# Kernel optimization log

Hardware: AMD Instinct MI355X
Metric: run time of the kernel (lower is better)

## Reference

```python
import jax, jax.numpy as jnp
import numpy as np
import math

K = 8          # wavelet order (k)
C = 64         # channels (c)
ICH = 512      # ich = c*k
ALPHA = 16     # fourier modes
BATCH, SEQ, NH, NE = 4, 3072, 8, 64   # x: [B, L, H, E], H*E == ICH


def _legendre_filters(k):
    # numpy port of FiSSM/FEDformer get_filter(base='legendre', k): PHI0=PHI1=I
    from numpy.polynomial import legendre as npl, polynomial as npp
    phi_c = np.zeros((k, k)); phi2_c = np.zeros((k, k))
    for ki in range(k):
        e = np.zeros(ki + 1); e[ki] = 1.0
        pc = npl.leg2poly(e)                                  # P_ki power coeffs
        p = npp.Polynomial(pc)(npp.Polynomial([-1.0, 2.0]))
        phi_c[ki, :len(p.coef)] = np.sqrt(2 * ki + 1) * p.coef
        p2 = npp.Polynomial(pc)(npp.Polynomial([-1.0, 4.0]))
        phi2_c[ki, :len(p2.coef)] = np.sqrt(2.0) * np.sqrt(2 * ki + 1) * p2.coef

    def _int_half(prod, upper_half):
        prod = prod.copy(); prod[np.abs(prod) < 1e-8] = 0
        n = np.arange(len(prod))
        w = (1 - np.power(0.5, 1 + n)) if upper_half else np.power(0.5, 1 + n)
        return (prod / (n + 1) * w).sum()

    psi1_c = np.zeros((k, k)); psi2_c = np.zeros((k, k))
    for ki in range(k):
        psi1_c[ki] = phi2_c[ki]
        for i in range(k):
            proj = _int_half(np.convolve(phi2_c[ki, :ki + 1], phi_c[i, :i + 1]), False)
            psi1_c[ki] -= proj * phi_c[i]
            psi2_c[ki] -= proj * phi_c[i]
        for j in range(ki):
            proj = _int_half(np.convolve(phi2_c[ki, :ki + 1], psi1_c[j]), False)
            psi1_c[ki] -= proj * psi1_c[j]
            psi2_c[ki] -= proj * psi2_c[j]
        norm1 = _int_half(np.convolve(psi1_c[ki], psi1_c[ki]), False)
        norm2 = _int_half(np.convolve(psi2_c[ki], psi2_c[ki]), True)
        nrm = np.sqrt(norm1 + norm2)
        psi1_c[ki] /= nrm; psi2_c[ki] /= nrm
        psi1_c[np.abs(psi1_c) < 1e-8] = 0; psi2_c[np.abs(psi2_c) < 1e-8] = 0

    nodes, weights = np.polynomial.legendre.leggauss(k)
    xm = (nodes + 1) / 2; wm = weights / 2     # Gauss-Legendre on [0,1]
    pv = np.polynomial.polynomial.polyval
    phi = lambda i, t: pv(t, phi_c[i])
    psi = lambda i, t: np.where(t <= 0.5, pv(t, psi1_c[i]), pv(t, psi2_c[i]))
    H0 = np.zeros((k, k)); H1 = np.zeros((k, k)); G0 = np.zeros((k, k)); G1 = np.zeros((k, k))
    r2 = 1 / np.sqrt(2)
    for ki in range(k):
        for kp in range(k):
            base = wm * phi(kp, xm)
            H0[ki, kp] = r2 * (base * phi(ki, xm / 2)).sum()
            G0[ki, kp] = r2 * (base * psi(ki, xm / 2)).sum()
            H1[ki, kp] = r2 * (base * phi(ki, (xm + 1) / 2)).sum()
            G1[ki, kp] = r2 * (base * psi(ki, (xm + 1) / 2)).sum()
    for M in (H0, H1, G0, G1):
        M[np.abs(M) < 1e-8] = 0
    ec_s = np.concatenate([H0.T, H1.T], 0).astype(np.float32)   # [2k, k]
    ec_d = np.concatenate([G0.T, G1.T], 0).astype(np.float32)
    rc_e = np.concatenate([H0, G0], 0).astype(np.float32)       # H0r=H0@I etc.
    rc_o = np.concatenate([H1, G1], 0).astype(np.float32)
    return ec_s, ec_d, rc_e, rc_o


def _skft(x, wr, wi):
    # sparseKernelFT2d: FFT-domain conv over the sequence axis, low `modes1` bins
    B, L, c, k = x.shape
    xv = x.reshape(B, L, c * k).transpose(0, 2, 1)     # [B, ck, L]
    xf = jnp.fft.rfft(xv)                              # [B, ck, L//2+1]
    nf = L // 2 + 1
    l = min(wr.shape[-1], nf)
    w = jax.lax.complex(wr[:, :, :l], wi[:, :, :l])
    out = jnp.einsum('bix,iox->box', xf[:, :, :l], w)
    out_ft = jnp.zeros((B, c * k, nf), dtype=out.dtype).at[:, :, :l].set(out)
    y = jnp.fft.irfft(out_ft, n=L)                     # torch default n == L (L even here)
    return y.transpose(0, 2, 1).reshape(B, L, c, k)


def _forward(x, Lk0_w, Lk0_b, Lk1_w, Lk1_b, T0_w, T0_b, Ar, Ai, Br, Bi, Cr, Ci, ec_s, ec_d, rc_e, rc_o):
    B, L, H, E = x.shape
    v = x.reshape(B, L, H * E) @ Lk0_w.T + Lk0_b       # Lk0: ich -> c*k
    v = v.reshape(B, L, C, K)
    # --- MWT_CZ2d (nCZ = 1, level offset self.L = 0) ---
    ns = int(math.floor(math.log2(L)))
    nl = 2 ** int(math.ceil(math.log2(L)))
    v = jnp.concatenate([v, v[:, :nl - L]], axis=1)    # circular-style pad to 2^ceil
    Ud, Us = [], []
    for _ in range(ns):                                # wavelet decompose
        xa = jnp.concatenate([v[:, ::2], v[:, 1::2]], axis=-1)   # [B, N/2, c, 2k]
        d = xa @ ec_d
        v = xa @ ec_s
        Ud.append(_skft(d, Ar, Ai) + _skft(v, Br, Bi))
        Us.append(_skft(d, Cr, Ci))
    v = v @ T0_w.T + T0_b                              # T0 on coarsest scale
    for i in range(ns - 1, -1, -1):                    # evenOdd reconstruct
        v = v + Us[i]
        ve = jnp.concatenate([v, Ud[i]], axis=-1)      # [B, N, c, 2k]
        xe = ve @ rc_e
        xo = ve @ rc_o
        v = jnp.stack([xe, xo], axis=2).reshape(xe.shape[0], 2 * xe.shape[1], C, K)
    v = v[:, :L]
    out = v.reshape(B, L, C * K) @ Lk1_w.T + Lk1_b     # Lk1: c*k -> ich
    return out.reshape(B, L, -1, E)


def setup_inputs():
    key = jax.random.key(0)
    ks = jax.random.split(key, 13)
    ck = C * K
    x = jax.random.normal(ks[0], (BATCH, SEQ, NH, NE), jnp.float32)
    l0 = 1.0 / math.sqrt(ICH)
    l1 = 1.0 / math.sqrt(ck)
    lt = 1.0 / math.sqrt(K)
    scale = 1.0 / (ck * ck)
    u = lambda k_, shp, lo, hi: jax.random.uniform(k_, shp, jnp.float32, lo, hi)
    inp = dict(
        x=x,
        Lk0_w=u(ks[1], (ck, ICH), -l0, l0), Lk0_b=u(ks[2], (ck,), -l0, l0),
        Lk1_w=u(ks[3], (ICH, ck), -l1, l1), Lk1_b=u(ks[4], (ICH,), -l1, l1),
        T0_w=u(ks[5], (K, K), -lt, lt), T0_b=u(ks[6], (K,), -lt, lt),
        Ar=scale * u(ks[7], (ck, ck, ALPHA), 0.0, 1.0), Ai=scale * u(ks[8], (ck, ck, ALPHA), 0.0, 1.0),
        Br=scale * u(ks[9], (ck, ck, ALPHA), 0.0, 1.0), Bi=scale * u(ks[10], (ck, ck, ALPHA), 0.0, 1.0),
        Cr=scale * u(ks[11], (ck, ck, ALPHA), 0.0, 1.0), Ci=scale * u(ks[12], (ck, ck, ALPHA), 0.0, 1.0),
    )
    ec_s, ec_d, rc_e, rc_o = _legendre_filters(K)
    inp.update(ec_s=jnp.asarray(ec_s), ec_d=jnp.asarray(ec_d),
               rc_e=jnp.asarray(rc_e), rc_o=jnp.asarray(rc_o))
    return inp


def reference(x, Lk0_w, Lk0_b, Lk1_w, Lk1_b, T0_w, T0_b, Ar, Ai, Br, Bi, Cr, Ci, ec_s, ec_d, rc_e, rc_o):
    return _forward(x, Lk0_w, Lk0_b, Lk1_w, Lk1_b, T0_w, T0_b,
                    Ar, Ai, Br, Bi, Cr, Ci, ec_s, ec_d, rc_e, rc_o)
```

## Files before the change

### kernel.cpp

```cpp
#include <hip/hip_runtime.h>

#define CKD 512
#define NROWS 44
#define XPLANE 360448

static __device__ __forceinline__ int imin(int a, int b) { return a < b ? a : b; }

typedef short bf16x8 __attribute__((ext_vector_type(8)));
typedef float f32x4 __attribute__((ext_vector_type(4)));
typedef unsigned int uint32;
typedef unsigned short ushort16;

static __device__ __forceinline__ unsigned int pk2(float a, float b) {
  unsigned int ua = __float_as_uint(a), ub = __float_as_uint(b);
  ua = (ua + 0x7fffu + ((ua >> 16) & 1u)) >> 16;
  ub = (ub + 0x7fffu + ((ub >> 16) & 1u)) >> 16;
  return ua | (ub << 16);
}

static __device__ __forceinline__ uint32 ror16(uint32 q) { return (q >> 16) | (q << 16); }

static __device__ __forceinline__ bf16x8 mk_neghi(uint32 q0, uint32 q1, uint32 q2, uint32 q3) {
  union { uint32 u[4]; bf16x8 h; } t;
  t.u[0] = q0 ^ 0x80000000u; t.u[1] = q1 ^ 0x80000000u;
  t.u[2] = q2 ^ 0x80000000u; t.u[3] = q3 ^ 0x80000000u;
  return t.h;
}
static __device__ __forceinline__ bf16x8 mk_swap(uint32 q0, uint32 q1, uint32 q2, uint32 q3) {
  union { uint32 u[4]; bf16x8 h; } t;
  t.u[0] = ror16(q0); t.u[1] = ror16(q1); t.u[2] = ror16(q2); t.u[3] = ror16(q3);
  return t.h;
}

__global__ __launch_bounds__(256) void k_cvt_x(
    const float* __restrict__ src, unsigned short* __restrict__ dst)
{
  int g = blockIdx.x * 256 + threadIdx.x;
  int row = g >> 6, c8 = (g & 63) << 3;
  int b = row >> 12, t = row & 4095;
  if (t >= 3072) t -= 3072;
  const float* s = src + ((size_t)(b * 3072 + t) << 9) + c8;
  float4 v0 = *(const float4*)s;
  float4 v1 = *(const float4*)(s + 4);
  uint4 o = make_uint4(pk2(v0.x, v0.y), pk2(v0.z, v0.w),
                       pk2(v1.x, v1.y), pk2(v1.z, v1.w));
  *(uint4*)(dst + ((size_t)row << 9) + c8) = o;
}

__global__ __launch_bounds__(256) void k_cvt_gen(
    const float* __restrict__ src, unsigned short* __restrict__ dst)
{
  int g = blockIdx.x * 256 + threadIdx.x;
  const float* s = src + ((size_t)g << 3);
  float4 v0 = *(const float4*)s;
  float4 v1 = *(const float4*)(s + 4);
  uint4 o = make_uint4(pk2(v0.x, v0.y), pk2(v0.z, v0.w),
                       pk2(v1.x, v1.y), pk2(v1.z, v1.w));
  *(uint4*)(dst + ((size_t)g << 3)) = o;
}

__global__ __launch_bounds__(256) void k_cvt_c(
    const float* __restrict__ src, unsigned short* __restrict__ dst)
{
  int g = blockIdx.x * 256 + threadIdx.x;
  int row = g >> 6, c8 = (g & 63) << 3;
  int b = row / 3072, t = row - b * 3072;
  const float* s = src + ((size_t)((b << 12) + t) << 9) + c8;
  float4 v0 = *(const float4*)s;
  float4 v1 = *(const float4*)(s + 4);
  uint4 o = make_uint4(pk2(v0.x, v0.y), pk2(v0.z, v0.w),
                       pk2(v1.x, v1.y), pk2(v1.z, v1.w));
  *(uint4*)(dst + ((size_t)row << 9) + c8) = o;
}

__global__ __launch_bounds__(256) void k_gemm_bf16(
    const unsigned short* __restrict__ A, const unsigned short* __restrict__ W,
    const float* __restrict__ bias, float* __restrict__ Out)
{
  __shared__ unsigned short As[128 * 40];
  __shared__ unsigned short Bs[128 * 40];
  const int tid = threadIdx.x;
  const int row = tid >> 1, half = tid & 1;
  const int bm0 = blockIdx.x << 7, bn0 = blockIdx.y << 7;
  const int wv = tid >> 6, l = tid & 63;
  const int wm0 = (wv & 1) << 6, wn0 = (wv >> 1) << 6;
  const int fr = l & 15, fq = l >> 4;

  const unsigned short* Ap = A + (size_t)(bm0 + row) * CKD + half * 16;
  const unsigned short* Wp = W + (size_t)(bn0 + row) * CKD + half * 16;

  f32x4 acc[4][4];
#pragma unroll
  for (int mt = 0; mt < 4; ++mt)
#pragma unroll
    for (int nt = 0; nt < 4; ++nt) {
      acc[mt][nt][0] = 0.f; acc[mt][nt][1] = 0.f;
      acc[mt][nt][2] = 0.f; acc[mt][nt][3] = 0.f;
    }

  for (int k0 = 0; k0 < CKD; k0 += 32) {
    uint4 av0 = *(const uint4*)(Ap + k0);
    uint4 av1 = *(const uint4*)(Ap + k0 + 8);
    uint4 bv0 = *(const uint4*)(Wp + k0);
    uint4 bv1 = *(const uint4*)(Wp + k0 + 8);
    __syncthreads();
    *(uint4*)&As[row * 40 + half * 16]     = av0;
    *(uint4*)&As[row * 40 + half * 16 + 8] = av1;
    *(uint4*)&Bs[row * 40 + half * 16]     = bv0;
    *(uint4*)&Bs[row * 40 + half * 16 + 8] = bv1;
    __syncthreads();
    bf16x8 af[4], bfr[4];
#pragma unroll
    for (int mt = 0; mt < 4; ++mt)
      af[mt] = *(const bf16x8*)&As[(wm0 + mt * 16 + fr) * 40 + fq * 8];
#pragma unroll
    for (int nt = 0; nt < 4; ++nt)
      bfr[nt] = *(const bf16x8*)&Bs[(wn0 + nt * 16 + fr) * 40 + fq * 8];
#pragma unroll
    for (int mt = 0; mt < 4; ++mt)
#pragma unroll
      for (int nt = 0; nt < 4; ++nt)
        acc[mt][nt] = __builtin_amdgcn_mfma_f32_16x16x32_bf16(
            af[mt], bfr[nt], acc[mt][nt], 0, 0, 0);
  }

#pragma unroll
  for (int nt = 0; nt < 4; ++nt) {
    int col = bn0 + wn0 + nt * 16 + fr;
    float bv = bias[col];
#pragma unroll
    for (int mt = 0; mt < 4; ++mt) {
      int r0 = bm0 + wm0 + mt * 16 + fq * 4;
#pragma unroll
      for (int rg = 0; rg < 4; ++rg)
        Out[(size_t)(r0 + rg) * CKD + col] = acc[mt][nt][rg] + bv;
    }
  }
}

__global__ __launch_bounds__(256) void k_decomp(
    const float* __restrict__ Vin, const float* __restrict__ ec_s,
    const float* __restrict__ ec_d, float* __restrict__ Dout,
    float* __restrict__ Vout, int Lout, int pin)
{
  __shared__ float Es[128], Ed[128];
  if (threadIdx.x < 128) Es[threadIdx.x] = ec_s[threadIdx.x];
  else Ed[threadIdx.x - 128] = ec_d[threadIdx.x - 128];
  __syncthreads();
  int g = blockIdx.x * 256 + threadIdx.x;
  if (g >= 4 * Lout * 64) return;
  int c = g & 63;
  int s = (g >> 6) % Lout;
  int b = g / (Lout << 6);
  const float* r0 = Vin + ((size_t)b * pin + 2 * s) * CKD + (c << 3);
  float a[16];
  float4 v0 = *(const float4*)r0;
  float4 v1 = *(const float4*)(r0 + 4);
  float4 v2 = *(const float4*)(r0 + CKD);
  float4 v3 = *(const float4*)(r0 + CKD + 4);
  a[0]=v0.x; a[1]=v0.y; a[2]=v0.z; a[3]=v0.w; a[4]=v1.x; a[5]=v1.y; a[6]=v1.z; a[7]=v1.w;
  a[8]=v2.x; a[9]=v2.y; a[10]=v2.z; a[11]=v2.w; a[12]=v3.x; a[13]=v3.y; a[14]=v3.z; a[15]=v3.w;
  float dv[8] = {}, vv[8] = {};
#pragma unroll
  for (int m = 0; m < 16; ++m)
#pragma unroll
    for (int k = 0; k < 8; ++k) {
      dv[k] += a[m] * Ed[m * 8 + k];
      vv[k] += a[m] * Es[m * 8 + k];
    }
  size_t orow = ((size_t)b * Lout + s) * CKD + (c << 3);
  *(float4*)(Dout + orow)     = make_float4(dv[0], dv[1], dv[2], dv[3]);
  *(float4*)(Dout + orow + 4) = make_float4(dv[4], dv[5], dv[6], dv[7]);
  *(float4*)(Vout + orow)     = make_float4(vv[0], vv[1], vv[2], vv[3]);
  *(float4*)(Vout + orow + 4) = make_float4(vv[4], vv[5], vv[6], vv[7]);
}

__global__ __launch_bounds__(256) void k_t0(
    const float* __restrict__ Vin, const float* __restrict__ T0w,
    const float* __restrict__ T0b, float* __restrict__ Out)
{
  int g = blockIdx.x * 256 + threadIdx.x;
  if (g >= 4 * 2 * 64) return;
  int c = g & 63;
  int t = (g >> 6) & 1;
  int b = g >> 7;
  const float* src = Vin + ((size_t)(b * 2 + t)) * CKD + (c << 3);
  float a[8];
  float4 v0 = *(const float4*)src;
  float4 v1 = *(const float4*)(src + 4);
  a[0]=v0.x; a[1]=v0.y; a[2]=v0.z; a[3]=v0.w; a[4]=v1.x; a[5]=v1.y; a[6]=v1.z; a[7]=v1.w;
  float o[8];
#pragma unroll
  for (int ko = 0; ko < 8; ++ko) {
    float sum = T0b[ko];
#pragma unroll
    for (int k = 0; k < 8; ++k) sum += a[k] * T0w[ko * 8 + k];
    o[ko] = sum;
  }
  float* dst = Out + ((size_t)(b * 2 + t)) * CKD + (c << 3);
  *(float4*)dst       = make_float4(o[0], o[1], o[2], o[3]);
  *(float4*)(dst + 4) = make_float4(o[4], o[5], o[6], o[7]);
}

__global__ __launch_bounds__(256) void k_fdft(
    const float* __restrict__ DD, const float* __restrict__ VD,
    float* __restrict__ XDre, float* __restrict__ XDim,
    float* __restrict__ XVre, float* __restrict__ XVim)
{
  __shared__ float2 tw[2048];
  int bx = blockIdx.x, j = 1;
  for (;;) {
    int c = (4096 >> j) >> 7; if (c < 1) c = 1;
    if (bx < c) break;
    bx -= c; ++j;
  }
  const int L = 4096 >> j;
  const int t0 = bx << 7;
  const int tcnt = imin(128, L - t0);
  const int b = blockIdx.y;
  const int z = blockIdx.z;
  const int r = (j - 1) * 4 + b;
  const float* src = (z ? VD : DD) +
      ((size_t)(4 * (4096 - (4096 >> (j - 1))) + b * L)) * CKD;
  float* dre = z ? XVre : XDre;
  float* dim_ = z ? XVim : XDim;

  for (int idx = threadIdx.x; idx < 2048; idx += 256) {
    int ff = idx >> 7, tl = idx & 127;
    int t = t0 + tl;
    int m = (2 * ff * t) & (2 * L - 1);
    float xang = (float)m / (float)L;
    tw[idx] = make_float2(cospif(xang), sinpif(xang));
  }
  __syncthreads();

  float ar[16][2] = {};
  float ai[16][2] = {};
  const float* sp = src + (size_t)t0 * CKD + (threadIdx.x << 1);
  for (int tl = 0; tl < tcnt; ++tl) {
    float2 xv = *(const float2*)sp;
    sp += CKD;
#pragma unroll
    for (int ff = 0; ff < 16; ++ff) {
      float2 cs = tw[(ff << 7) + tl];
      ar[ff][0] += xv.x * cs.x; ar[ff][1] += xv.y * cs.x;
      ai[ff][0] -= xv.x * cs.y; ai[ff][1] -= xv.y * cs.y;
    }
  }
  const int i0 = threadIdx.x << 1;
#pragma unroll
  for (int ff = 0; ff < 16; ++ff) {
    size_t bidx = ((size_t)ff * NROWS + r) * CKD + i0;
    atomicAdd(&dre[bidx], ar[ff][0]);
    atomicAdd(&dre[bidx + 1], ar[ff][1]);
    atomicAdd(&dim_[bidx], ai[ff][0]);
    atomicAdd(&dim_[bidx + 1], ai[ff][1]);
  }
}

__global__ __launch_bounds__(256) void k_transw6b(
    const float* __restrict__ sAr, const float* __restrict__ sAi,
    const float* __restrict__ sBr, const float* __restrict__ sBi,
    const float* __restrict__ sCr, const float* __restrict__ sCi,
    uint2* __restrict__ W4b, uint32* __restrict__ W2b)
{
  int g = blockIdx.x * 256 + threadIdx.x;
  float ar[16], ai[16], br[16], bi[16], cr[16], ci[16];
  const size_t sb = (size_t)g * 16;
#pragma unroll
  for (int q = 0; q < 4; ++q) {
    float4 t;
    t = *(const float4*)(sAr + sb + q * 4); ar[q*4]=t.x; ar[q*4+1]=t.y; ar[q*4+2]=t.z; ar[q*4+3]=t.w;
    t = *(const float4*)(sAi + sb + q * 4); ai[q*4]=t.x; ai[q*4+1]=t.y; ai[q*4+2]=t.z; ai[q*4+3]=t.w;
    t = *(const float4*)(sBr + sb + q * 4); br[q*4]=t.x; br[q*4+1]=t.y; br[q*4+2]=t.z; br[q*4+3]=t.w;
    t = *(const float4*)(sBi + sb + q * 4); bi[q*4]=t.x; bi[q*4+1]=t.y; bi[q*4+2]=t.z; bi[q*4+3]=t.w;
    t = *(const float4*)(sCr + sb + q * 4); cr[q*4]=t.x; cr[q*4+1]=t.y; cr[q*4+2]=t.z; cr[q*4+3]=t.w;
    t = *(const float4*)(sCi + sb + q * 4); ci[q*4]=t.x; ci[q*4+1]=t.y; ci[q*4+2]=t.z; ci[q*4+3]=t.w;
  }
#pragma unroll
  for (int f = 0; f < 16; ++f) {
    size_t e = ((size_t)f << 18) + g;
    W4b[e] = make_uint2(pk2(ar[f], ai[f]), pk2(br[f], bi[f]));
    W2b[e] = pk2(cr[f], ci[f]);
  }
}

__global__ __launch_bounds__(256) void k_packA(
    const float* __restrict__ XDre, const float* __restrict__ XDim,
    const float* __restrict__ XVre, const float* __restrict__ XVim,
    unsigned short* __restrict__ Aud, unsigned short* __restrict__ Aus)
{
  int g = blockIdx.x * 256 + threadIdx.x;
  int f = g / 6144;
  int rem = g - f * 6144;
  int r = rem >> 7, iq = rem & 127;
  uint4 w0 = make_uint4(0,0,0,0), w1 = w0, wu = w0;
  if (r < NROWS) {
    size_t base = ((size_t)f * NROWS + r) * CKD + (iq << 2);
    float4 dre = *(const float4*)(XDre + base);
    float4 dim_ = *(const float4*)(XDim + base);
    float4 vre = *(const float4*)(XVre + base);
    float4 vim = *(const float4*)(XVim + base);
    w0 = make_uint4(pk2(dre.x, dim_.x), pk2(vre.x, vim.x),
                    pk2(dre.y, dim_.y), pk2(vre.y, vim.y));
    w1 = make_uint4(pk2(dre.z, dim_.z), pk2(vre.z, vim.z),
                    pk2(dre.w, dim_.w), pk2(vre.w, vim.w));
    wu = make_uint4(pk2(dre.x, dim_.x), pk2(dre.y, dim_.y),
                    pk2(dre.z, dim_.z), pk2(dre.w, dim_.w));
  }
  size_t du = ((size_t)f * 48 + r) * 2048 + (iq << 4);
  *(uint4*)(Aud + du)     = w0;
  *(uint4*)(Aud + du + 8) = w1;
  *(uint4*)(Aus + ((size_t)f * 48 + r) * 1024 + (iq << 3)) = wu;
}

__global__ __launch_bounds__(256) void k_mixmm(
    const uint2* __restrict__ W4b, const uint32* __restrict__ W2b,
    const unsigned short* __restrict__ Aud, const unsigned short* __restrict__ Aus,
    float* __restrict__ Part)
{
  __shared__ __attribute__((aligned(16))) uint2 sBud[16 * 130];
  __shared__ __attribute__((aligned(16))) uint32 sBus[16 * 132];
  __shared__ __attribute__((aligned(16))) unsigned short sAud[48 * 72];
  __shared__ __attribute__((aligned(16))) unsigned short sAus[48 * 40];

  const int f = blockIdx.x;
  const int o0 = blockIdx.y << 7;
  const int is = blockIdx.z;
  const int i0 = is << 7;
  const int tid = threadIdx.x;
  const int w = tid >> 6, l = tid & 63;
  const int fr = l & 15, fq = l >> 4;
  const int ow0 = w << 5;

  const uint2* gW4 = W4b + ((size_t)f << 18);
  const uint32* gW2 = W2b + ((size_t)f << 18);
  const unsigned short* gAud = Aud + (size_t)f * 48 * 2048;
  const unsigned short* gAus = Aus + (size_t)f * 48 * 1024;

  f32x4 aUd[3][2][2], aUs[3][2][2];
#pragma unroll
  for (int m = 0; m < 3; ++m)
#pragma unroll
    for (int ot = 0; ot < 2; ++ot)
#pragma unroll
      for (int cp = 0; cp < 2; ++cp) {
        aUd[m][ot][cp][0]=0.f; aUd[m][ot][cp][1]=0.f; aUd[m][ot][cp][2]=0.f; aUd[m][ot][cp][3]=0.f;
        aUs[m][ot][cp][0]=0.f; aUs[m][ot][cp][1]=0.f; aUs[m][ot][cp][2]=0.f; aUs[m][ot][cp][3]=0.f;
      }

  for (int ic = 0; ic < 8; ++ic) {
    const int ig = i0 + (ic << 4);
    __syncthreads();
#pragma unroll
    for (int n = 0; n < 4; ++n) {
      int q = tid + (n << 8);
      int il = q >> 6, op = (q & 63) << 1;
      uint4 v = *(const uint4*)(gW4 + (size_t)(ig + il) * 512 + o0 + op);
      *(uint4*)&sBud[il * 130 + op] = v;
    }
#pragma unroll
    for (int n = 0; n < 2; ++n) {
      int q = tid + (n << 8);
      int il = q >> 5, oq = (q & 31) << 2;
      uint4 v = *(const uint4*)(gW2 + (size_t)(ig + il) * 512 + o0 + oq);
      *(uint4*)&sBus[il * 132 + oq] = v;
    }
    {
      int q = tid;
      int m = q >> 3, k8 = (q & 7) << 3;
      uint4 v = *(const uint4*)(gAud + (size_t)m * 2048 + (is << 9) + (ic << 6) + k8);
      *(uint4*)&sAud[m * 72 + k8] = v;
      q = tid + 256;
      if (q < 384) {
        m = q >> 3; k8 = (q & 7) << 3;
        uint4 v2 = *(const uint4*)(gAud + (size_t)m * 2048 + (is << 9) + (ic << 6) + k8);
        *(uint4*)&sAud[m * 72 + k8] = v2;
      }
    }
    if (tid < 192) {
      int m = tid >> 2, k8 = (tid & 3) << 3;
      uint4 v = *(const uint4*)(gAus + (size_t)m * 1024 + (is << 8) + (ic << 5) + k8);
      *(uint4*)&sAus[m * 40 + k8] = v;
    }
    __syncthreads();

#pragma unroll
    for (int ks = 0; ks < 2; ++ks) {
      bf16x8 af[3];
#pragma unroll
      for (int m = 0; m < 3; ++m)
        af[m] = *(const bf16x8*)&sAud[(m * 16 + fr) * 72 + (ks << 5) + (fq << 3)];
#pragma unroll
      for (int ot = 0; ot < 2; ++ot) {
        int ol = ow0 + (ot << 4) + fr;
        int il = (ks << 3) + (fq << 1);
        uint2 qa = sBud[il * 130 + ol];
        uint2 qb = sBud[(il + 1) * 130 + ol];
        bf16x8 b0 = mk_neghi(qa.x, qa.y, qb.x, qb.y);
        bf16x8 b1 = mk_swap(qa.x, qa.y, qb.x, qb.y);
#pragma unroll
        for (int m = 0; m < 3; ++m) {
          aUd[m][ot][0] = __builtin_amdgcn_mfma_f32_16x16x32_bf16(af[m], b0, aUd[m][ot][0], 0, 0, 0);
          aUd[m][ot][1] = __builtin_amdgcn_mfma_f32_16x16x32_bf16(af[m], b1, aUd[m][ot][1], 0, 0, 0);
        }
      }
    }
    {
      bf16x8 af[3];
#pragma unroll
      for (int m = 0; m < 3; ++m)
        af[m] = *(const bf16x8*)&sAus[(m * 16 + fr) * 40 + (fq << 3)];
#pragma unroll
      for (int ot = 0; ot < 2; ++ot) {
        int ol = ow0 + (ot << 4) + fr;
        int il = fq << 2;
        uint32 q0 = sBus[(il + 0) * 132 + ol];
        uint32 q1 = sBus[(il + 1) * 132 + ol];
        uint32 q2 = sBus[(il + 2) * 132 + ol];
        uint32 q3 = sBus[(il + 3) * 132 + ol];
        bf16x8 b0 = mk_neghi(q0, q1, q2, q3);
        bf16x8 b1 = mk_swap(q0, q1, q2, q3);
#pragma unroll
        for (int m = 0; m < 3; ++m) {
          aUs[m][ot][0] = __builtin_amdgcn_mfma_f32_16x16x32_bf16(af[m], b0, aUs[m][ot][0], 0, 0, 0);
          aUs[m][ot][1] = __builtin_amdgcn_mfma_f32_16x16x32_bf16(af[m], b1, aUs[m][ot][1], 0, 0, 0);
        }
      }
    }
  }

  float* P = Part + (size_t)is * 4 * XPLANE;
#pragma unroll
  for (int m = 0; m < 3; ++m) {
#pragma unroll
    for (int reg = 0; reg < 4; ++reg) {
      int r = m * 16 + (fq << 2) + reg;
      if (r < NROWS) {
        size_t rb = ((size_t)f * NROWS + r) * CKD;
#pragma unroll
        for (int ot = 0; ot < 2; ++ot) {
          int col = o0 + ow0 + (ot << 4) + fr;
          P[0 * XPLANE + rb + col] = aUd[m][ot][0][reg];
          P[1 * XPLANE + rb + col] = aUd[m][ot][1][reg];
          P[2 * XPLANE + rb + col] = aUs[m][ot][0][reg];
          P[3 * XPLANE + rb + col] = aUs[m][ot][1][reg];
        }
      }
    }
  }
}

__global__ __launch_bounds__(256) void k_reduce4(
    const float* __restrict__ Part,
    float* __restrict__ UdFre, float* __restrict__ UdFim,
    float* __restrict__ UsFre, float* __restrict__ UsFim)
{
  int idx = blockIdx.x * 256 + threadIdx.x;
  if (idx >= XPLANE) return;
  float s0 = 0.f, s1 = 0.f, s2 = 0.f, s3 = 0.f;
#pragma unroll
  for (int is = 0; is < 4; ++is) {
    const float* p = Part + (size_t)is * 4 * XPLANE;
    s0 += p[0 * XPLANE + idx];
    s1 += p[1 * XPLANE + idx];
    s2 += p[2 * XPLANE + idx];
    s3 += p[3 * XPLANE + idx];
  }
  UdFre[idx] = s0; UdFim[idx] = s1; UsFre[idx] = s2; UsFim[idx] = s3;
}

__global__ __launch_bounds__(512) void k_mix_fb(
    const float* __restrict__ XDre, const float* __restrict__ XDim,
    const float* __restrict__ XVre, const float* __restrict__ XVim,
    const float* __restrict__ war, const float* __restrict__ wai,
    const float* __restrict__ wbr, const float* __restrict__ wbi,
    const float* __restrict__ wcr, const float* __restrict__ wci,
    float* __restrict__ UdFre, float* __restrict__ UdFim,
    float* __restrict__ UsFre, float* __restrict__ UsFim)
{
  const int f = blockIdx.x;
  const int ot = blockIdx.y;
  const int lane = threadIdx.x & 63;
  const int rg = threadIdx.x >> 6;
  const int rbase = (rg < 4) ? rg * 6 : 24 + (rg - 4) * 5;
  const int rcnt = (rg < 4) ? 6 : 5;
  const int o0 = (ot << 7) + lane;
  __shared__ float4 sx[NROWS * 64];
  float udr[6][2] = {}, udi[6][2] = {}, usr[6][2] = {}, usi[6][2] = {};
  for (int i0 = 0; i0 < 512; i0 += 64) {
    __syncthreads();
    for (int idx = threadIdx.x; idx < NROWS * 64; idx += 512) {
      int r = idx >> 6, il = idx & 63;
      size_t xb = ((size_t)f * NROWS + r) * CKD + i0 + il;
      sx[idx] = make_float4(XDre[xb], XDim[xb], XVre[xb], XVim[xb]);
    }
    __syncthreads();
    for (int ii = 0; ii < 64; ++ii) {
      int i = i0 + ii;
      size_t wo = ((((size_t)i << 9) + o0) << 4) + f;
      float4 wa0 = make_float4(war[wo], wai[wo], wbr[wo], wbi[wo]);
      float2 wc0 = make_float2(wcr[wo], wci[wo]);
      size_t w1 = wo + (64u << 4);
      float4 wa1 = make_float4(war[w1], wai[w1], wbr[w1], wbi[w1]);
      float2 wc1 = make_float2(wcr[w1], wci[w1]);
#pragma unroll
      for (int rr = 0; rr < 6; ++rr) {
        if (rr < rcnt) {
          float4 xv = sx[((rbase + rr) << 6) + ii];
          udr[rr][0] += xv.x * wa0.x - xv.y * wa0.y + xv.z * wa0.z - xv.w * wa0.w;
          udi[rr][0] += xv.x * wa0.y + xv.y * wa0.x + xv.z * wa0.w + xv.w * wa0.z;
          usr[rr][0] += xv.x * wc0.x - xv.y * wc0.y;
          usi[rr][0] += xv.x * wc0.y + xv.y * wc0.x;
          udr[rr][1] += xv.x * wa1.x - xv.y * wa1.y + xv.z * wa1.z - xv.w * wa1.w;
          udi[rr][1] += xv.x * wa1.y + xv.y * wa1.x + xv.z * wa1.w + xv.w * wa1.z;
          usr[rr][1] += xv.x * wc1.x - xv.y * wc1.y;
          usi[rr][1] += xv.x * wc1.y + xv.y * wc1.x;
        }
      }
    }
  }
#pragma unroll
  for (int rr = 0; rr < 6; ++rr) {
    if (rr < rcnt) {
      size_t rb_ = ((size_t)f * NROWS + rbase + rr) * CKD;
      UdFre[rb_ + o0] = udr[rr][0];      UdFre[rb_ + o0 + 64] = udr[rr][1];
      UdFim[rb_ + o0] = udi[rr][0];      UdFim[rb_ + o0 + 64] = udi[rr][1];
      UsFre[rb_ + o0] = usr[rr][0];      UsFre[rb_ + o0 + 64] = usr[rr][1];
      UsFim[rb_ + o0] = usi[rr][0];      UsFim[rb_ + o0 + 64] = usi[rr][1];
    }
  }
}

__global__ __launch_bounds__(256) void k_idft(
    const float* __restrict__ UdFre, const float* __restrict__ UdFim,
    const float* __restrict__ UsFre, const float* __restrict__ UsFim,
    float* __restrict__ UdT, float* __restrict__ UsT)
{
  __shared__ float2 tw[128];
  int bx = blockIdx.x, j = 1;
  for (;;) {
    int c = (4096 >> j) >> 3; if (c < 1) c = 1;
    if (bx < c) break;
    bx -= c; ++j;
  }
  const int L = 4096 >> j;
  const int l = imin(16, (L >> 1) + 1);
  const int t0 = bx << 3;
  const int b = blockIdx.y;
  const int r = (j - 1) * 4 + b;
  if (threadIdx.x < 128) {
    int ff = threadIdx.x >> 3, tl = threadIdx.x & 7;
    int t = t0 + tl;
    int m = (2 * ff * t) & (2 * L - 1);
    float xang = (float)m / (float)L;
    float wgt = (ff == 0 || 2 * ff == L) ? 1.0f : 2.0f;
    float sc = wgt / (float)L;
    tw[threadIdx.x] = make_float2(cospif(xang) * sc, sinpif(xang) * sc);
  }
  __syncthreads();
  const int o = threadIdx.x << 1;
  float2 ud[8], us[8];
#pragma unroll
  for (int tl = 0; tl < 8; ++tl) { ud[tl] = make_float2(0.f, 0.f); us[tl] = make_float2(0.f, 0.f); }
  for (int ff = 0; ff < l; ++ff) {
    size_t bidx = ((size_t)ff * NROWS + r) * CKD + o;
    float2 er = *(const float2*)(UdFre + bidx);
    float2 ei = *(const float2*)(UdFim + bidx);
    float2 sr = *(const float2*)(UsFre + bidx);
    float2 si = *(const float2*)(UsFim + bidx);
#pragma unroll
    for (int tl = 0; tl < 8; ++tl) {
      float2 cs = tw[(ff << 3) + tl];
      ud[tl].x += er.x * cs.x - ei.x * cs.y;
      ud[tl].y += er.y * cs.x - ei.y * cs.y;
      us[tl].x += sr.x * cs.x - si.x * cs.y;
      us[tl].y += sr.y * cs.x - si.y * cs.y;
    }
  }
  int tmax = imin(8, L - t0);
  size_t obase = ((size_t)(4 * (4096 - (4096 >> (j - 1))) + b * L + t0)) * CKD + o;
  for (int tl = 0; tl < tmax; ++tl) {
    *(float2*)(UdT + obase + (size_t)tl * CKD) = ud[tl];
    *(float2*)(UsT + obase + (size_t)tl * CKD) = us[tl];
  }
}

__global__ __launch_bounds__(256) void k_recon(
    const float* __restrict__ Vcur, const float* __restrict__ UdT,
    const float* __restrict__ UsT, const float* __restrict__ rc_e,
    const float* __restrict__ rc_o, float* __restrict__ Vnext,
    int Lc, int abase)
{
  __shared__ float Re[128], Ro[128];
  if (threadIdx.x < 128) Re[threadIdx.x] = rc_e[threadIdx.x];
  else Ro[threadIdx.x - 128] = rc_o[threadIdx.x - 128];
  __syncthreads();
  int g = blockIdx.x * 256 + threadIdx.x;
  if (g >= 4 * Lc * 64) return;
  int c = g & 63;
  int s = (g >> 6) % Lc;
  int b = g / (Lc << 6);
  size_t vrow = ((size_t)b * Lc + s) * CKD + (c << 3);
  size_t arow = ((size_t)abase + (size_t)b * Lc + s) * CKD + (c << 3);
  float a[16];
  {
    float4 t0_ = *(const float4*)(Vcur + vrow);
    float4 t1_ = *(const float4*)(Vcur + vrow + 4);
    float4 u0 = *(const float4*)(UsT + arow);
    float4 u1 = *(const float4*)(UsT + arow + 4);
    a[0]=t0_.x+u0.x; a[1]=t0_.y+u0.y; a[2]=t0_.z+u0.z; a[3]=t0_.w+u0.w;
    a[4]=t1_.x+u1.x; a[5]=t1_.y+u1.y; a[6]=t1_.z+u1.z; a[7]=t1_.w+u1.w;
    float4 d0 = *(const float4*)(UdT + arow);
    float4 d1 = *(const float4*)(UdT + arow + 4);
    a[8]=d0.x; a[9]=d0.y; a[10]=d0.z; a[11]=d0.w;
    a[12]=d1.x; a[13]=d1.y; a[14]=d1.z; a[15]=d1.w;
  }
  float xe[8] = {}, xo[8] = {};
#pragma unroll
  for (int m = 0; m < 16; ++m)
#pragma unroll
    for (int k = 0; k < 8; ++k) {
      xe[k] += a[m] * Re[m * 8 + k];
      xo[k] += a[m] * Ro[m * 8 + k];
    }
  size_t orow = ((size_t)b * (Lc << 1) + (s << 1)) * CKD + (c << 3);
  *(float4*)(Vnext + orow)           = make_float4(xe[0], xe[1], xe[2], xe[3]);
  *(float4*)(Vnext + orow + 4)       = make_float4(xe[4], xe[5], xe[6], xe[7]);
  *(float4*)(Vnext + orow + CKD)     = make_float4(xo[0], xo[1], xo[2], xo[3]);
  *(float4*)(Vnext + orow + CKD + 4) = make_float4(xo[4], xo[5], xo[6], xo[7]);
}

extern "C" void kernel_launch(void* const* d_in, const int* in_sizes, int n_in,
                              void* d_out, int out_size, void* d_ws, size_t ws_size,
                              hipStream_t stream)
{
  const float* x     = (const float*)d_in[0];
  const float* Lk0_w = (const float*)d_in[1];
  const float* Lk0_b = (const float*)d_in[2];
  const float* Lk1_w = (const float*)d_in[3];
  const float* Lk1_b = (const float*)d_in[4];
  const float* T0_w  = (const float*)d_in[5];
  const float* T0_b  = (const float*)d_in[6];
  const float* Ar = (const float*)d_in[7];
  const float* Ai = (const float*)d_in[8];
  const float* Br = (const float*)d_in[9];
  const float* Bi = (const float*)d_in[10];
  const float* Cr = (const float*)d_in[11];
  const float* Ci = (const float*)d_in[12];
  const float* ec_s = (const float*)d_in[13];
  const float* ec_d = (const float*)d_in[14];
  const float* rc_e = (const float*)d_in[15];
  const float* rc_o = (const float*)d_in[16];
  float* out = (float*)d_out;

  float* w = (float*)d_ws;
  float* V0 = w;   w += (size_t)4 * 4096 * 512;
  float* VD = w;   w += (size_t)4 * 4094 * 512;
  float* DD = w;   w += (size_t)4 * 4094 * 512;
  float* RB = w;   w += (size_t)4 * 4096 * 512;
  float* XDre = w; w += XPLANE;
  float* XDim = w; w += XPLANE;
  float* XVre = w; w += XPLANE;
  float* XVim = w; w += XPLANE;
  float* UdFre = w; w += XPLANE;
  float* UdFim = w; w += XPLANE;
  float* UsFre = w; w += XPLANE;
  float* UsFim = w; w += XPLANE;
  float* WT = w;
  float* RA = V0;
  float* UdT = DD;
  float* UsT = VD;
  float* Part = RB;

  unsigned short* Xb  = (unsigned short*)RB;
  unsigned short* Cb  = (unsigned short*)DD;
  unsigned short* Wb0 = (unsigned short*)UdFre;
  unsigned short* Wb1 = (unsigned short*)UdFre;

  const size_t BASE_FLOATS = 36421632ull;
  const size_t WT_FLOATS   = 25165824ull;
  if (ws_size < BASE_FLOATS * 4) return;
  const bool use_wt = ws_size >= (BASE_FLOATS + WT_FLOATS) * 4;
  uint2*  W4b = (uint2*)WT;
  uint32* W2b = (uint32*)(WT + 8388608ull);
  unsigned short* AudP = (unsigned short*)(WT + 12582912ull);
  unsigned short* AusP = (unsigned short*)(WT + 13369344ull);

  k_cvt_x<<<dim3(4096), dim3(256), 0, stream>>>(x, Xb);
  k_cvt_gen<<<dim3(128), dim3(256), 0, stream>>>(Lk0_w, Wb0);
  k_gemm_bf16<<<dim3(128, 4), dim3(256), 0, stream>>>(Xb, Wb0, Lk0_b, V0);

  for (int j = 1; j <= 11; ++j) {
    int Lout = 4096 >> j;
    int pin = 4096 >> (j - 1);
    const float* vin = (j == 1)
        ? V0
        : VD + (size_t)4 * (4096 - (4096 >> (j - 2))) * 512;
    size_t base = (size_t)4 * (4096 - (4096 >> (j - 1))) * 512;
    k_decomp<<<dim3(Lout), dim3(256), 0, stream>>>(vin, ec_s, ec_d,
                                                   DD + base, VD + base, Lout, pin);
  }

  k_t0<<<dim3(2), dim3(256), 0, stream>>>(VD + (size_t)4 * 4092 * 512, T0_w, T0_b, RA);

  hipMemsetAsync(XDre, 0, (size_t)4 * XPLANE * 4, stream);

  if (use_wt)
    k_transw6b<<<dim3(1024), dim3(256), 0, stream>>>(Ar, Ai, Br, Bi, Cr, Ci, W4b, W2b);

  k_fdft<<<dim3(37, 4, 2), dim3(256), 0, stream>>>(DD, VD, XDre, XDim, XVre, XVim);

  if (use_wt) {
    k_packA<<<dim3(384), dim3(256), 0, stream>>>(XDre, XDim, XVre, XVim, AudP, AusP);
    k_mixmm<<<dim3(16, 4, 4), dim3(256), 0, stream>>>(W4b, W2b, AudP, AusP, Part);
    k_reduce4<<<dim3((XPLANE + 255) / 256), dim3(256), 0, stream>>>(
        Part, UdFre, UdFim, UsFre, UsFim);
  } else {
    k_mix_fb<<<dim3(16, 4), dim3(512), 0, stream>>>(
        XDre, XDim, XVre, XVim, Ar, Ai, Br, Bi, Cr, Ci,
        UdFre, UdFim, UsFre, UsFim);
  }

  k_idft<<<dim3(513, 4), dim3(256), 0, stream>>>(UdFre, UdFim, UsFre, UsFim, UdT, UsT);

  float* cur = RA;
  float* nxt = RB;
  for (int j = 11; j >= 1; --j) {
    int Lc = 4096 >> j;
    int abase = 4 * (4096 - (4096 >> (j - 1)));
    k_recon<<<dim3(Lc), dim3(256), 0, stream>>>(cur, UdT, UsT, rc_e, rc_o, nxt, Lc, abase);
    float* t = cur; cur = nxt; nxt = t;
  }

  k_cvt_c<<<dim3(3072), dim3(256), 0, stream>>>(cur, Cb);
  k_cvt_gen<<<dim3(128), dim3(256), 0, stream>>>(Lk1_w, Wb1);
  k_gemm_bf16<<<dim3(96, 4), dim3(256), 0, stream>>>(Cb, Wb1, Lk1_b, out);
}
```

Baseline: 522.8 us.

## Fuse multi-level wavelet decomposition and reconstruction into shared-memory tree kernels

Replaces the 11 per-level decomposition launches and 11 per-level reconstruction launches with three launches each. Each block keeps several consecutive levels of intermediate coefficients in shared memory, which cuts launch overhead and global round-trips. The forward DFT kernel is retiled to 64-timestep chunks, which gives more blocks, and it prefetches the next input row. The tail kernels covering the coarsest levels run with only 4 blocks, and the larger shared-memory buffers lower occupancy.

```diff
diff --git a/kernel.cpp b/kernel.cpp
--- a/kernel.cpp
+++ b/kernel.cpp
@@ -9,7 +9,6 @@
 typedef short bf16x8 __attribute__((ext_vector_type(8)));
 typedef float f32x4 __attribute__((ext_vector_type(4)));
 typedef unsigned int uint32;
-typedef unsigned short ushort16;
 
 static __device__ __forceinline__ unsigned int pk2(float a, float b) {
   unsigned int ua = __float_as_uint(a), ub = __float_as_uint(b);
@@ -138,41 +137,69 @@
   }
 }
 
-__global__ __launch_bounds__(256) void k_decomp(
+__global__ __launch_bounds__(256) void k_decomp_tree(
     const float* __restrict__ Vin, const float* __restrict__ ec_s,
-    const float* __restrict__ ec_d, float* __restrict__ Dout,
-    float* __restrict__ Vout, int Lout, int pin)
+    const float* __restrict__ ec_d, float* __restrict__ DD,
+    float* __restrict__ VD, int j0, int NL, int pin)
 {
   __shared__ float Es[128], Ed[128];
-  if (threadIdx.x < 128) Es[threadIdx.x] = ec_s[threadIdx.x];
-  else Ed[threadIdx.x - 128] = ec_d[threadIdx.x - 128];
+  __shared__ float bufA[16 * 512];
+  __shared__ float bufB[8 * 512];
+  const int tid = threadIdx.x;
+  if (tid < 128) Es[tid] = ec_s[tid];
+  else Ed[tid - 128] = ec_d[tid - 128];
+  const int b = blockIdx.y;
+  const int t0 = blockIdx.x << 4;
+
+  const float* src = Vin + ((size_t)b * pin + t0) * CKD;
+  for (int q = tid; q < 16 * 128; q += 256) {
+    int rr = q >> 7, c4 = (q & 127) << 2;
+    *(float4*)&bufA[rr * 512 + c4] = *(const float4*)(src + (size_t)rr * CKD + c4);
+  }
   __syncthreads();
-  int g = blockIdx.x * 256 + threadIdx.x;
-  if (g >= 4 * Lout * 64) return;
-  int c = g & 63;
-  int s = (g >> 6) % Lout;
-  int b = g / (Lout << 6);
-  const float* r0 = Vin + ((size_t)b * pin + 2 * s) * CKD + (c << 3);
-  float a[16];
-  float4 v0 = *(const float4*)r0;
-  float4 v1 = *(const float4*)(r0 + 4);
-  float4 v2 = *(const float4*)(r0 + CKD);
-  float4 v3 = *(const float4*)(r0 + CKD + 4);
-  a[0]=v0.x; a[1]=v0.y; a[2]=v0.z; a[3]=v0.w; a[4]=v1.x; a[5]=v1.y; a[6]=v1.z; a[7]=v1.w;
-  a[8]=v2.x; a[9]=v2.y; a[10]=v2.z; a[11]=v2.w; a[12]=v3.x; a[13]=v3.y; a[14]=v3.z; a[15]=v3.w;
-  float dv[8] = {}, vv[8] = {};
-#pragma unroll
-  for (int m = 0; m < 16; ++m)
-#pragma unroll
-    for (int k = 0; k < 8; ++k) {
-      dv[k] += a[m] * Ed[m * 8 + k];
-      vv[k] += a[m] * Es[m * 8 + k];
-    }
-  size_t orow = ((size_t)b * Lout + s) * CKD + (c << 3);
-  *(float4*)(Dout + orow)     = make_float4(dv[0], dv[1], dv[2], dv[3]);
-  *(float4*)(Dout + orow + 4) = make_float4(dv[4], dv[5], dv[6], dv[7]);
-  *(float4*)(Vout + orow)     = make_float4(vv[0], vv[1], vv[2], vv[3]);
-  *(float4*)(Vout + orow + 4) = make_float4(vv[4], vv[5], vv[6], vv[7]);
+
+  float* rd = bufA;
+  float* wr = bufB;
+  for (int lv = 0; lv < NL; ++lv) {
+    const int j = j0 + lv;
+    const int Lout = 4096 >> j;
+    const int rows = 8 >> lv;
+    const int sb = t0 >> (lv + 1);
+    const size_t base = 4ull * (4096 - (4096 >> (j - 1))) * CKD;
+    float* Dp = DD + base;
+    float* Vp = VD + base;
+    for (int task = tid; task < rows * 64; task += 256) {
+      int s = task >> 6, c = task & 63;
+      const float* r0p = rd + (2 * s) * 512 + (c << 3);
+      float a[16];
+      float4 v0 = *(const float4*)r0p;
+      float4 v1 = *(const float4*)(r0p + 4);
+      float4 v2 = *(const float4*)(r0p + 512);
+      float4 v3 = *(const float4*)(r0p + 516);
+      a[0]=v0.x; a[1]=v0.y; a[2]=v0.z; a[3]=v0.w; a[4]=v1.x; a[5]=v1.y; a[6]=v1.z; a[7]=v1.w;
+      a[8]=v2.x; a[9]=v2.y; a[10]=v2.z; a[11]=v2.w; a[12]=v3.x; a[13]=v3.y; a[14]=v3.z; a[15]=v3.w;
+      float dv[8] = {}, vv[8] = {};
+#pragma unroll
+      for (int m = 0; m < 16; ++m)
+#pragma unroll
+        for (int k = 0; k < 8; ++k) {
+          dv[k] += a[m] * Ed[m * 8 + k];
+          vv[k] += a[m] * Es[m * 8 + k];
+        }
+      size_t orow = ((size_t)b * Lout + sb + s) * CKD + (c << 3);
+      *(float4*)(Dp + orow)     = make_float4(dv[0], dv[1], dv[2], dv[3]);
+      *(float4*)(Dp + orow + 4) = make_float4(dv[4], dv[5], dv[6], dv[7]);
+      *(float4*)(Vp + orow)     = make_float4(vv[0], vv[1], vv[2], vv[3]);
+      *(float4*)(Vp + orow + 4) = make_float4(vv[4], vv[5], vv[6], vv[7]);
+      if (lv + 1 < NL) {
+        float* wp = wr + s * 512 + (c << 3);
+        *(float4*)wp       = make_float4(vv[0], vv[1], vv[2], vv[3]);
+        *(float4*)(wp + 4) = make_float4(vv[4], vv[5], vv[6], vv[7]);
+      }
+    }
+    __syncthreads();
+    float* t = rd; rd = wr; wr = t;
+  }
 }
 
 __global__ __launch_bounds__(256) void k_t0(
@@ -207,16 +234,16 @@
     float* __restrict__ XDre, float* __restrict__ XDim,
     float* __restrict__ XVre, float* __restrict__ XVim)
 {
-  __shared__ float2 tw[2048];
+  __shared__ float2 tw[1024];
   int bx = blockIdx.x, j = 1;
   for (;;) {
-    int c = (4096 >> j) >> 7; if (c < 1) c = 1;
+    int c = (4096 >> j) >> 6; if (c < 1) c = 1;
     if (bx < c) break;
     bx -= c; ++j;
   }
   const int L = 4096 >> j;
-  const int t0 = bx << 7;
-  const int tcnt = imin(128, L - t0);
+  const int t0 = bx << 6;
+  const int tcnt = imin(64, L - t0);
   const int b = blockIdx.y;
   const int z = blockIdx.z;
   const int r = (j - 1) * 4 + b;
@@ -225,8 +252,8 @@
   float* dre = z ? XVre : XDre;
   float* dim_ = z ? XVim : XDim;
 
-  for (int idx = threadIdx.x; idx < 2048; idx += 256) {
-    int ff = idx >> 7, tl = idx & 127;
+  for (int idx = threadIdx.x; idx < 1024; idx += 256) {
+    int ff = idx >> 6, tl = idx & 63;
     int t = t0 + tl;
     int m = (2 * ff * t) & (2 * L - 1);
     float xang = (float)m / (float)L;
@@ -237,12 +264,13 @@
   float ar[16][2] = {};
   float ai[16][2] = {};
   const float* sp = src + (size_t)t0 * CKD + (threadIdx.x << 1);
+  float2 nxt = *(const float2*)sp;
   for (int tl = 0; tl < tcnt; ++tl) {
-    float2 xv = *(const float2*)sp;
-    sp += CKD;
+    float2 xv = nxt;
+    if (tl + 1 < tcnt) nxt = *(const float2*)(sp + (size_t)(tl + 1) * CKD);
 #pragma unroll
     for (int ff = 0; ff < 16; ++ff) {
-      float2 cs = tw[(ff << 7) + tl];
+      float2 cs = tw[(ff << 6) + tl];
       ar[ff][0] += xv.x * cs.x; ar[ff][1] += xv.y * cs.x;
       ai[ff][0] -= xv.x * cs.y; ai[ff][1] -= xv.y * cs.y;
     }
@@ -586,49 +614,77 @@
   }
 }
 
-__global__ __launch_bounds__(256) void k_recon(
-    const float* __restrict__ Vcur, const float* __restrict__ UdT,
+__global__ __launch_bounds__(256) void k_recon_tree(
+    const float* __restrict__ Vin, const float* __restrict__ UdT,
     const float* __restrict__ UsT, const float* __restrict__ rc_e,
-    const float* __restrict__ rc_o, float* __restrict__ Vnext,
-    int Lc, int abase)
+    const float* __restrict__ rc_o, float* __restrict__ Vout,
+    int j0, int NL, int ir, int pin, int pout)
 {
   __shared__ float Re[128], Ro[128];
-  if (threadIdx.x < 128) Re[threadIdx.x] = rc_e[threadIdx.x];
-  else Ro[threadIdx.x - 128] = rc_o[threadIdx.x - 128];
+  __shared__ float bufA[16 * 512];
+  __shared__ float bufB[16 * 512];
+  const int tid = threadIdx.x;
+  if (tid < 128) Re[tid] = rc_e[tid];
+  else Ro[tid - 128] = rc_o[tid - 128];
+  const int b = blockIdx.y;
+  const int r0 = blockIdx.x * ir;
+
+  for (int q = tid; q < ir * 128; q += 256) {
+    int rr = q >> 7, c4 = (q & 127) << 2;
+    *(float4*)&bufA[rr * 512 + c4] =
+        *(const float4*)(Vin + ((size_t)b * pin + r0 + rr) * CKD + c4);
+  }
   __syncthreads();
-  int g = blockIdx.x * 256 + threadIdx.x;
-  if (g >= 4 * Lc * 64) return;
-  int c = g & 63;
-  int s = (g >> 6) % Lc;
-  int b = g / (Lc << 6);
-  size_t vrow = ((size_t)b * Lc + s) * CKD + (c << 3);
-  size_t arow = ((size_t)abase + (size_t)b * Lc + s) * CKD + (c << 3);
-  float a[16];
-  {
-    float4 t0_ = *(const float4*)(Vcur + vrow);
-    float4 t1_ = *(const float4*)(Vcur + vrow + 4);
-    float4 u0 = *(const float4*)(UsT + arow);
-    float4 u1 = *(const float4*)(UsT + arow + 4);
-    a[0]=t0_.x+u0.x; a[1]=t0_.y+u0.y; a[2]=t0_.z+u0.z; a[3]=t0_.w+u0.w;
-    a[4]=t1_.x+u1.x; a[5]=t1_.y+u1.y; a[6]=t1_.z+u1.z; a[7]=t1_.w+u1.w;
-    float4 d0 = *(const float4*)(UdT + arow);
-    float4 d1 = *(const float4*)(UdT + arow + 4);
-    a[8]=d0.x; a[9]=d0.y; a[10]=d0.z; a[11]=d0.w;
-    a[12]=d1.x; a[13]=d1.y; a[14]=d1.z; a[15]=d1.w;
-  }
-  float xe[8] = {}, xo[8] = {};
-#pragma unroll
-  for (int m = 0; m < 16; ++m)
-#pragma unroll
-    for (int k = 0; k < 8; ++k) {
-      xe[k] += a[m] * Re[m * 8 + k];
-      xo[k] += a[m] * Ro[m * 8 + k];
-    }
-  size_t orow = ((size_t)b * (Lc << 1) + (s << 1)) * CKD + (c << 3);
-  *(float4*)(Vnext + orow)           = make_float4(xe[0], xe[1], xe[2], xe[3]);
-  *(float4*)(Vnext + orow + 4)       = make_float4(xe[4], xe[5], xe[6], xe[7]);
-  *(float4*)(Vnext + orow + CKD)     = make_float4(xo[0], xo[1], xo[2], xo[3]);
-  *(float4*)(Vnext + orow + CKD + 4) = make_float4(xo[4], xo[5], xo[6], xo[7]);
+
+  float* rd = bufA;
+  float* wr = bufB;
+  int rows = ir;
+  for (int m = 0; m < NL; ++m) {
+    const int j = j0 - m;
+    const int Lc = 4096 >> j;
+    const size_t ab = 4ull * (4096 - (4096 >> (j - 1))) * CKD;
+    const int g0 = r0 << m;
+    for (int task = tid; task < rows * 64; task += 256) {
+      int s = task >> 6, c = task & 63;
+      size_t arow = ab + ((size_t)b * Lc + g0 + s) * CKD + (c << 3);
+      const float* vp = rd + s * 512 + (c << 3);
+      float a[16];
+      {
+        float4 t0_ = *(const float4*)vp;
+        float4 t1_ = *(const float4*)(vp + 4);
+        float4 u0 = *(const float4*)(UsT + arow);
+        float4 u1 = *(const float4*)(UsT + arow + 4);
+        a[0]=t0_.x+u0.x; a[1]=t0_.y+u0.y; a[2]=t0_.z+u0.z; a[3]=t0_.w+u0.w;
+        a[4]=t1_.x+u1.x; a[5]=t1_.y+u1.y; a[6]=t1_.z+u1.z; a[7]=t1_.w+u1.w;
+        float4 d0 = *(const float4*)(UdT + arow);
+        float4 d1 = *(const float4*)(UdT + arow + 4);
+        a[8]=d0.x; a[9]=d0.y; a[10]=d0.z; a[11]=d0.w;
+        a[12]=d1.x; a[13]=d1.y; a[14]=d1.z; a[15]=d1.w;
+      }
+      float xe[8] = {}, xo[8] = {};
+#pragma unroll
+      for (int mm = 0; mm < 16; ++mm)
+#pragma unroll
+        for (int k = 0; k < 8; ++k) {
+          xe[k] += a[mm] * Re[mm * 8 + k];
+          xo[k] += a[mm] * Ro[mm * 8 + k];
+        }
+      float* we = wr + (2 * s) * 512 + (c << 3);
+      *(float4*)we         = make_float4(xe[0], xe[1], xe[2], xe[3]);
+      *(float4*)(we + 4)   = make_float4(xe[4], xe[5], xe[6], xe[7]);
+      *(float4*)(we + 512) = make_float4(xo[0], xo[1], xo[2], xo[3]);
+      *(float4*)(we + 516) = make_float4(xo[4], xo[5], xo[6], xo[7]);
+    }
+    __syncthreads();
+    float* t = rd; rd = wr; wr = t;
+    rows <<= 1;
+  }
+
+  for (int q = tid; q < rows * 128; q += 256) {
+    int rr = q >> 7, c4 = (q & 127) << 2;
+    *(float4*)(Vout + ((size_t)b * pout + (r0 << NL) + rr) * CKD + c4) =
+        *(const float4*)&rd[rr * 512 + c4];
+  }
 }
 
 extern "C" void kernel_launch(void* const* d_in, const int* in_sizes, int n_in,
@@ -669,6 +725,8 @@
   float* UsFim = w; w += XPLANE;
   float* WT = w;
   float* RA = V0;
+  float* SA = V0 + 4096;
+  float* SB = V0 + 4096 + 32768;
   float* UdT = DD;
   float* UsT = VD;
   float* Part = RB;
@@ -691,16 +749,12 @@
   k_cvt_gen<<<dim3(128), dim3(256), 0, stream>>>(Lk0_w, Wb0);
   k_gemm_bf16<<<dim3(128, 4), dim3(256), 0, stream>>>(Xb, Wb0, Lk0_b, V0);
 
-  for (int j = 1; j <= 11; ++j) {
-    int Lout = 4096 >> j;
-    int pin = 4096 >> (j - 1);
-    const float* vin = (j == 1)
-        ? V0
-        : VD + (size_t)4 * (4096 - (4096 >> (j - 2))) * 512;
-    size_t base = (size_t)4 * (4096 - (4096 >> (j - 1))) * 512;
-    k_decomp<<<dim3(Lout), dim3(256), 0, stream>>>(vin, ec_s, ec_d,
-                                                   DD + base, VD + base, Lout, pin);
-  }
+  k_decomp_tree<<<dim3(256, 4), dim3(256), 0, stream>>>(
+      V0, ec_s, ec_d, DD, VD, 1, 4, 4096);
+  k_decomp_tree<<<dim3(16, 4), dim3(256), 0, stream>>>(
+      VD + 4ull * 3584 * 512, ec_s, ec_d, DD, VD, 5, 4, 256);
+  k_decomp_tree<<<dim3(1, 4), dim3(256), 0, stream>>>(
+      VD + 4ull * 4064 * 512, ec_s, ec_d, DD, VD, 9, 3, 16);
 
   k_t0<<<dim3(2), dim3(256), 0, stream>>>(VD + (size_t)4 * 4092 * 512, T0_w, T0_b, RA);
 
@@ -709,7 +763,7 @@
   if (use_wt)
     k_transw6b<<<dim3(1024), dim3(256), 0, stream>>>(Ar, Ai, Br, Bi, Cr, Ci, W4b, W2b);
 
-  k_fdft<<<dim3(37, 4, 2), dim3(256), 0, stream>>>(DD, VD, XDre, XDim, XVre, XVim);
+  k_fdft<<<dim3(68, 4, 2), dim3(256), 0, stream>>>(DD, VD, XDre, XDim, XVre, XVim);
 
   if (use_wt) {
     k_packA<<<dim3(384), dim3(256), 0, stream>>>(XDre, XDim, XVre, XVim, AudP, AusP);
@@ -724,16 +778,14 @@
 
   k_idft<<<dim3(513, 4), dim3(256), 0, stream>>>(UdFre, UdFim, UsFre, UsFim, UdT, UsT);
 
-  float* cur = RA;
-  float* nxt = RB;
-  for (int j = 11; j >= 1; --j) {
-    int Lc = 4096 >> j;
-    int abase = 4 * (4096 - (4096 >> (j - 1)));
-    k_recon<<<dim3(Lc), dim3(256), 0, stream>>>(cur, UdT, UsT, rc_e, rc_o, nxt, Lc, abase);
-    float* t = cur; cur = nxt; nxt = t;
-  }
-
-  k_cvt_c<<<dim3(3072), dim3(256), 0, stream>>>(cur, Cb);
+  k_recon_tree<<<dim3(1, 4), dim3(256), 0, stream>>>(
+      RA, UdT, UsT, rc_e, rc_o, SA, 11, 3, 2, 2, 16);
+  k_recon_tree<<<dim3(16, 4), dim3(256), 0, stream>>>(
+      SA, UdT, UsT, rc_e, rc_o, SB, 8, 4, 1, 16, 256);
+  k_recon_tree<<<dim3(256, 4), dim3(256), 0, stream>>>(
+      SB, UdT, UsT, rc_e, rc_o, RB, 4, 4, 1, 256, 4096);
+
+  k_cvt_c<<<dim3(3072), dim3(256), 0, stream>>>(RB, Cb);
   k_cvt_gen<<<dim3(128), dim3(256), 0, stream>>>(Lk1_w, Wb1);
   k_gemm_bf16<<<dim3(96, 4), dim3(256), 0, stream>>>(Cb, Wb1, Lk1_b, out);
 }
```

Measured after the change: 512.8 us. No clear change (-1.9%).
